# Performance work log

Hardware: AMD Instinct MI355X
Metric: run time of the kernel (lower is better)

Reference implementation:

```python
import jax, jax.numpy as jnp
import numpy as np

N, E, G, D, C = 100000, 1600000, 128, 64, 10  # nodes, edges, graphs, feat dim, classes


def setup_inputs() -> dict:
    key = jax.random.key(0)
    ks = jax.random.split(key, 14)
    s = 0.05
    return {
        "x": jax.random.normal(ks[0], (N, D), jnp.float32),
        # edge update MLP: concat(h_src,h_dst) -> hidden -> message (dim D to allow u_mul_e)
        "We1": jax.random.normal(ks[1], (2 * D, D), jnp.float32) * s,
        "be1": jnp.zeros((D,), jnp.float32),
        "We2": jax.random.normal(ks[2], (D, D), jnp.float32) * s,
        "be2": jnp.zeros((D,), jnp.float32),
        # node update MLP (hidden_dim -> hidden_dim)
        "Wn": jax.random.normal(ks[3], (D, D), jnp.float32) * s,
        "bn": jnp.zeros((D,), jnp.float32),
        # attention-pooling gate Linear(hidden_dim, 1)
        "Wg": jax.random.normal(ks[4], (D, 1), jnp.float32) * s,
        "bg": jnp.zeros((1,), jnp.float32),
        # final classifier
        "Wfc": jax.random.normal(ks[5], (D, C), jnp.float32) * s,
        "bfc": jnp.zeros((C,), jnp.float32),
        # graph structure
        "src": jax.random.randint(ks[6], (E,), 0, N),
        "dst": jax.random.randint(ks[7], (E,), 0, N),
        "graph_ids": jnp.sort(jax.random.randint(ks[8], (N,), 0, G)),
    }


def reference(x, We1, be1, We2, be2, Wn, bn, Wg, bg, Wfc, bfc, src, dst, graph_ids):
    h = x  # [N, D]
    # apply_edges: edge MLP on (h_src, h_dst) -> message m per edge  [E, D]
    e_in = jnp.concatenate([h[src], h[dst]], axis=-1)  # [E, 2D]
    m = jax.nn.relu(e_in @ We1 + be1) @ We2 + be2
    # update_all: u_mul_e('h','m') then sum-reduce onto destination nodes
    h_neigh = jax.ops.segment_sum(h[src] * m, dst, num_segments=N)  # [N, D]
    # apply_nodes: node MLP
    h2 = jax.nn.relu(h_neigh @ Wn + bn)  # [N, D]
    # GlobalAttentionPooling: per-graph softmax over node gates, weighted sum
    gate = h2 @ Wg + bg  # [N, 1]
    gmax = jax.ops.segment_max(gate, graph_ids, num_segments=G)  # [G, 1]
    a = jnp.exp(gate - gmax[graph_ids])
    denom = jax.ops.segment_sum(a, graph_ids, num_segments=G)  # [G, 1]
    a = a / denom[graph_ids]
    pooled = jax.ops.segment_sum(a * h2, graph_ids, num_segments=G)  # [G, D]
    return pooled @ Wfc + bfc  # [G, C]
```

## Files before the change

kernel.cpp:

```cpp
#include <hip/hip_runtime.h>
#include <hip/hip_bf16.h>

#define D 64
#define BSH 6
#define BNODES 64
#define NBMAX 2048
#define EB 4096

typedef _Float16 f16;
typedef _Float16 f16x4 __attribute__((ext_vector_type(4)));
typedef _Float16 f16x8 __attribute__((ext_vector_type(8)));
typedef float f32x4 __attribute__((ext_vector_type(4)));

__device__ __forceinline__ int sw7(int m, int k) {
    return (m << 7) + (((k >> 3) ^ (m & 7)) << 3) + (k & 7);
}
__device__ __forceinline__ int sw6(int m, int k) {
    return (m << 6) + ((((k >> 3) ^ (m & 7)) & 7) << 3) + (k & 7);
}

__global__ __launch_bounds__(256) void bucket_hist(
    const int* __restrict__ dst, int* __restrict__ bhist, int E, int NB)
{
    __shared__ int lhist[NBMAX];
    int tid = threadIdx.x;
    for (int b = tid; b < NB; b += 256) lhist[b] = 0;
    __syncthreads();
    int base = blockIdx.x * EB;
#pragma unroll
    for (int r = 0; r < EB / 256; ++r) {
        int e = base + r * 256 + tid;
        if (e < E) atomicAdd(&lhist[dst[e] >> BSH], 1);
    }
    __syncthreads();
    for (int b = tid; b < NB; b += 256) {
        int v = lhist[b];
        if (v) atomicAdd(&bhist[b], v);
    }
}

__global__ __launch_bounds__(256) void bucket_scan(
    const int* __restrict__ bhist, int* __restrict__ boff,
    int* __restrict__ bcursor, int NB)
{
    __shared__ int lds[256];
    int tid = threadIdx.x;
    int chunk = (NB + 255) / 256;
    int b0 = tid * chunk;
    int b1 = min(b0 + chunk, NB);
    int s = 0;
    for (int b = b0; b < b1; ++b) s += bhist[b];
    lds[tid] = s;
    __syncthreads();
    for (int d2 = 1; d2 < 256; d2 <<= 1) {
        int v = (tid >= d2) ? lds[tid - d2] : 0;
        __syncthreads();
        lds[tid] += v;
        __syncthreads();
    }
    int run = (tid == 0) ? 0 : lds[tid - 1];
    for (int b = b0; b < b1; ++b) {
        boff[b] = run;
        bcursor[b] = run;
        run += bhist[b];
    }
    if (tid == 255) boff[NB] = lds[255];
}

__global__ __launch_bounds__(256) void bucket_fill(
    const int* __restrict__ dst, const int* __restrict__ src,
    int* __restrict__ bcursor, int2* __restrict__ eix, int E, int NB)
{
    __shared__ int lhist[NBMAX];
    __shared__ int lcur[NBMAX];
    int tid = threadIdx.x;
    for (int b = tid; b < NB; b += 256) lhist[b] = 0;
    __syncthreads();
    int base = blockIdx.x * EB;
    int dv[EB / 256];
#pragma unroll
    for (int r = 0; r < EB / 256; ++r) {
        int e = base + r * 256 + tid;
        dv[r] = (e < E) ? dst[e] : -1;
        if (dv[r] >= 0) atomicAdd(&lhist[dv[r] >> BSH], 1);
    }
    __syncthreads();
    for (int b = tid; b < NB; b += 256) {
        int v = lhist[b];
        lcur[b] = v ? atomicAdd(&bcursor[b], v) : 0;
    }
    __syncthreads();
#pragma unroll
    for (int r = 0; r < EB / 256; ++r) {
        int e = base + r * 256 + tid;
        if (dv[r] >= 0) {
            int p = atomicAdd(&lcur[dv[r] >> BSH], 1);
            eix[p] = make_int2(src[e], dv[r]);
        }
    }
}

__global__ __launch_bounds__(256) void bucket_sort(
    const int2* __restrict__ eix, const int* __restrict__ boff,
    int2* __restrict__ eix2, int NB)
{
    __shared__ int h64[BNODES];
    __shared__ int cur64[BNODES];
    int bk = blockIdx.x;
    int s = boff[bk], e = boff[bk + 1];
    int tid = threadIdx.x;
    int nbase = bk << BSH;

    if (tid < BNODES) h64[tid] = 0;
    __syncthreads();
    for (int i = s + tid; i < e; i += 256)
        atomicAdd(&h64[eix[i].y - nbase], 1);
    __syncthreads();
    if (tid < BNODES) {
        int v = h64[tid];
        int inc = v;
        for (int d2 = 1; d2 < BNODES; d2 <<= 1) {
            int t = __shfl_up(inc, d2);
            if (tid >= d2) inc += t;
        }
        cur64[tid] = inc - v;
    }
    __syncthreads();
    for (int i = s + tid; i < e; i += 256) {
        int2 ed = eix[i];
        int slot = atomicAdd(&cur64[ed.y - nbase], 1);
        eix2[s + slot] = ed;
    }
}

__global__ __launch_bounds__(256, 2) void edge_mfma_kernel(
    const float* __restrict__ x,
    const float* __restrict__ We1, const float* __restrict__ be1,
    const float* __restrict__ We2, const float* __restrict__ be2,
    const int2* __restrict__ eix,
    float* __restrict__ hneigh, int N, int E, int T)
{
    __shared__ __attribute__((aligned(16))) float XCs[4][16 * 68];
    __shared__ __attribute__((aligned(16))) f16   Hbs[4][16 * 64];
    __shared__ int edsts[4][16];

    const int tid  = threadIdx.x;
    const int w    = tid >> 6;
    const int lane = tid & 63;
    const int l15  = lane & 15;
    const int quad = lane >> 4;

    float* XC  = XCs[w];
    f16*   Hb  = Hbs[w];
    int*   edst = edsts[w];

    f16x8 wb1[4][4];
#pragma unroll
    for (int kt = 0; kt < 4; ++kt)
#pragma unroll
        for (int nf = 0; nf < 4; ++nf) {
            int n = nf * 16 + l15;
#pragma unroll
            for (int j = 0; j < 8; ++j)
                wb1[kt][nf][j] = (f16)We1[(kt * 32 + quad * 8 + j) * 64 + n];
        }
    f16x8 wb2[2][4];
#pragma unroll
    for (int kt = 0; kt < 2; ++kt)
#pragma unroll
        for (int nf = 0; nf < 4; ++nf) {
            int n = nf * 16 + l15;
#pragma unroll
            for (int j = 0; j < 8; ++j)
                wb2[kt][nf][j] = (f16)We2[(kt * 32 + quad * 8 + j) * 64 + n];
        }

    float b1v[4], b2v[4];
#pragma unroll
    for (int nf = 0; nf < 4; ++nf) {
        b1v[nf] = be1[nf * 16 + l15];
        b2v[nf] = be2[nf * 16 + l15];
    }

    const int wid = blockIdx.x * 4 + w;
    const int nw  = gridDim.x * 4;

    int2 peC = eix[min(wid * 16 + l15, E - 1)];
    float4 s0, s1, s2, s3, d0v, d1v, d2v, d3v;
    {
        const float* ps = x + (size_t)peC.x * D;
        const float* pd = x + (size_t)peC.y * D;
        s0  = *(const float4*)(ps + quad * 8);
        s1  = *(const float4*)(ps + quad * 8 + 4);
        s2  = *(const float4*)(ps + 32 + quad * 8);
        s3  = *(const float4*)(ps + 32 + quad * 8 + 4);
        d0v = *(const float4*)(pd + quad * 8);
        d1v = *(const float4*)(pd + quad * 8 + 4);
        d2v = *(const float4*)(pd + 32 + quad * 8);
        d3v = *(const float4*)(pd + 32 + quad * 8 + 4);
    }
    int2 peN = eix[min((wid + nw) * 16 + l15, E - 1)];

    for (int tile = wid; tile < T; tile += nw) {
        const int e0 = tile * 16;

        int prevD = (e0 > 0)      ? eix[e0 - 1].y  : -2;
        int nextD = (e0 + 16 < E) ? eix[e0 + 16].y : -2;

        *(float4*)&XC[l15 * 68 + quad * 8]          = s0;
        *(float4*)&XC[l15 * 68 + quad * 8 + 4]      = s1;
        *(float4*)&XC[l15 * 68 + 32 + quad * 8]     = s2;
        *(float4*)&XC[l15 * 68 + 32 + quad * 8 + 4] = s3;
        if (quad == 0) edst[l15] = (e0 + l15 < E) ? peC.y : N;

        f16x8 ah[4];
        ah[0][0]=(f16)s0.x; ah[0][1]=(f16)s0.y; ah[0][2]=(f16)s0.z; ah[0][3]=(f16)s0.w;
        ah[0][4]=(f16)s1.x; ah[0][5]=(f16)s1.y; ah[0][6]=(f16)s1.z; ah[0][7]=(f16)s1.w;
        ah[1][0]=(f16)s2.x; ah[1][1]=(f16)s2.y; ah[1][2]=(f16)s2.z; ah[1][3]=(f16)s2.w;
        ah[1][4]=(f16)s3.x; ah[1][5]=(f16)s3.y; ah[1][6]=(f16)s3.z; ah[1][7]=(f16)s3.w;
        ah[2][0]=(f16)d0v.x; ah[2][1]=(f16)d0v.y; ah[2][2]=(f16)d0v.z; ah[2][3]=(f16)d0v.w;
        ah[2][4]=(f16)d1v.x; ah[2][5]=(f16)d1v.y; ah[2][6]=(f16)d1v.z; ah[2][7]=(f16)d1v.w;
        ah[3][0]=(f16)d2v.x; ah[3][1]=(f16)d2v.y; ah[3][2]=(f16)d2v.z; ah[3][3]=(f16)d2v.w;
        ah[3][4]=(f16)d3v.x; ah[3][5]=(f16)d3v.y; ah[3][6]=(f16)d3v.z; ah[3][7]=(f16)d3v.w;

        float4 t0, t1, t2, t3, u0, u1, u2, u3;
        int2 peN2;
        {
            const float* ps2 = x + (size_t)peN.x * D;
            const float* pd2 = x + (size_t)peN.y * D;
            t0 = *(const float4*)(ps2 + quad * 8);
            t1 = *(const float4*)(ps2 + quad * 8 + 4);
            t2 = *(const float4*)(ps2 + 32 + quad * 8);
            t3 = *(const float4*)(ps2 + 32 + quad * 8 + 4);
            u0 = *(const float4*)(pd2 + quad * 8);
            u1 = *(const float4*)(pd2 + quad * 8 + 4);
            u2 = *(const float4*)(pd2 + 32 + quad * 8);
            u3 = *(const float4*)(pd2 + 32 + quad * 8 + 4);
            peN2 = eix[min((tile + 2 * nw) * 16 + l15, E - 1)];
        }

        f32x4 acc[4] = {{0.f,0.f,0.f,0.f},{0.f,0.f,0.f,0.f},
                        {0.f,0.f,0.f,0.f},{0.f,0.f,0.f,0.f}};
#pragma unroll
        for (int kt = 0; kt < 4; ++kt)
#pragma unroll
            for (int nf = 0; nf < 4; ++nf)
                acc[nf] = __builtin_amdgcn_mfma_f32_16x16x32_f16(
                    ah[kt], wb1[kt][nf], acc[nf], 0, 0, 0);

#pragma unroll
        for (int nf = 0; nf < 4; ++nf)
#pragma unroll
            for (int i2 = 0; i2 < 4; ++i2)
                Hb[sw6(quad * 4 + i2, nf * 16 + l15)] =
                    (f16)fmaxf(acc[nf][i2] + b1v[nf], 0.f);

        f32x4 dd[4] = {{0.f,0.f,0.f,0.f},{0.f,0.f,0.f,0.f},
                       {0.f,0.f,0.f,0.f},{0.f,0.f,0.f,0.f}};
#pragma unroll
        for (int kt = 0; kt < 2; ++kt) {
            f16x8 ah2 = *(const f16x8*)&Hb[sw6(l15, kt * 32 + quad * 8)];
#pragma unroll
            for (int nf = 0; nf < 4; ++nf)
                dd[nf] = __builtin_amdgcn_mfma_f32_16x16x32_f16(
                    ah2, wb2[kt][nf], dd[nf], 0, 0, 0);
        }

#pragma unroll
        for (int nf = 0; nf < 4; ++nf)
#pragma unroll
            for (int i2 = 0; i2 < 4; ++i2) {
                int a = (quad * 4 + i2) * 68 + nf * 16 + l15;
                XC[a] = (dd[nf][i2] + b2v[nf]) * XC[a];
            }

        {
            int j = lane;
            float a = 0.f;
            int cur = edst[0];
            int runStart = 0;
#pragma unroll
            for (int ii = 0; ii < 16; ++ii) {
                a += XC[ii * 68 + j];
                int nxt = (ii < 15) ? edst[ii + 1] : -3;
                if (nxt != cur) {
                    bool firstRun = (runStart == 0);
                    bool lastRun = (ii == 15) || (nxt >= N);
                    bool complete = (!firstRun || prevD != cur) &&
                                    (!lastRun || nextD != cur);
                    if (complete) hneigh[(size_t)cur * D + j] = a;
                    else atomicAdd(&hneigh[(size_t)cur * D + j], a);
                    a = 0.f; cur = nxt; runStart = ii + 1;
                }
            }
        }

        s0 = t0; s1 = t1; s2 = t2; s3 = t3;
        d0v = u0; d1v = u1; d2v = u2; d3v = u3;
        peC = peN; peN = peN2;
    }
}

__global__ __launch_bounds__(256, 4) void node_mfma_kernel(
    float* __restrict__ h,
    const float* __restrict__ Wn, const float* __restrict__ bn,
    const float* __restrict__ Wg, const float* __restrict__ bg,
    float* __restrict__ gate, int N, int T)
{
    __shared__ __attribute__((aligned(16))) f16 ANhi[64 * 64];
    __shared__ __attribute__((aligned(16))) f16 ANlo[64 * 64];

    const int tid = threadIdx.x;
    const int w = tid >> 6;
    const int lane = tid & 63;
    const int l15 = lane & 15;
    const int quad = lane >> 4;
    const int m0 = w * 16;

    f16x8 wn[2][4];
#pragma unroll
    for (int kt = 0; kt < 2; ++kt)
#pragma unroll
        for (int nf = 0; nf < 4; ++nf) {
            int n = nf * 16 + l15;
#pragma unroll
            for (int j = 0; j < 8; ++j)
                wn[kt][nf][j] = (f16)Wn[(kt * 32 + quad * 8 + j) * 64 + n];
        }

    float bnv[4], wgv[4];
#pragma unroll
    for (int nt = 0; nt < 4; ++nt) {
        bnv[nt] = bn[nt * 16 + l15];
        wgv[nt] = Wg[nt * 16 + l15];
    }
    const float bgv = bg[0];

    for (int tile = blockIdx.x; tile < T; tile += gridDim.x) {
        const int t0 = tile * 64;

        {
            int i = tid >> 2;
            int q = tid & 3;
            int node = min(t0 + i, N - 1);
            const float* p = h + (size_t)node * D + q * 16;
#pragma unroll
            for (int r = 0; r < 4; ++r) {
                float4 v = *(const float4*)(p + r * 4);
                int k = q * 16 + r * 4;
                f16x4 hv, lv;
                hv[0] = (f16)v.x; lv[0] = (f16)(v.x - (float)hv[0]);
                hv[1] = (f16)v.y; lv[1] = (f16)(v.y - (float)hv[1]);
                hv[2] = (f16)v.z; lv[2] = (f16)(v.z - (float)hv[2]);
                hv[3] = (f16)v.w; lv[3] = (f16)(v.w - (float)hv[3]);
                *(f16x4*)&ANhi[sw6(i, k)] = hv;
                *(f16x4*)&ANlo[sw6(i, k)] = lv;
            }
        }
        __syncthreads();

        f32x4 cacc[4] = {{0.f,0.f,0.f,0.f},{0.f,0.f,0.f,0.f},{0.f,0.f,0.f,0.f},{0.f,0.f,0.f,0.f}};
#pragma unroll
        for (int kt = 0; kt < 2; ++kt) {
            int k = kt * 32 + quad * 8;
            f16x8 ah = *(const f16x8*)&ANhi[sw6(m0 + l15, k)];
            f16x8 al = *(const f16x8*)&ANlo[sw6(m0 + l15, k)];
#pragma unroll
            for (int nf = 0; nf < 4; ++nf) {
                cacc[nf] = __builtin_amdgcn_mfma_f32_16x16x32_f16(ah, wn[kt][nf], cacc[nf], 0, 0, 0);
                cacc[nf] = __builtin_amdgcn_mfma_f32_16x16x32_f16(al, wn[kt][nf], cacc[nf], 0, 0, 0);
            }
        }
        __syncthreads();

        float gpart[4] = {0.f, 0.f, 0.f, 0.f};
#pragma unroll
        for (int nt = 0; nt < 4; ++nt) {
            int n = nt * 16 + l15;
#pragma unroll
            for (int i2 = 0; i2 < 4; ++i2) {
                int m = t0 + m0 + quad * 4 + i2;
                float v = fmaxf(cacc[nt][i2] + bnv[nt], 0.f);
                if (m < N) h[(size_t)m * D + n] = v;
                gpart[i2] += v * wgv[nt];
            }
        }
#pragma unroll
        for (int s = 1; s < 16; s <<= 1) {
#pragma unroll
            for (int i2 = 0; i2 < 4; ++i2) gpart[i2] += __shfl_xor(gpart[i2], s);
        }
        if (l15 == 0) {
#pragma unroll
            for (int i2 = 0; i2 < 4; ++i2) {
                int m = t0 + m0 + quad * 4 + i2;
                if (m < N) gate[m] = gpart[i2] + bgv;
            }
        }
    }
}

__global__ __launch_bounds__(256) void pool_kernel(
    const float* __restrict__ h2,
    const float* __restrict__ gate,
    const int* __restrict__ gid,
    const float* __restrict__ Wfc, const float* __restrict__ bfc,
    float* __restrict__ out, int N, int C)
{
    int g = blockIdx.x;
    int tid = threadIdx.x;

    int lo = 0, hi = N;
    while (lo < hi) { int mid = (lo + hi) >> 1; if (gid[mid] < g) lo = mid + 1; else hi = mid; }
    int s = lo;
    hi = N;
    while (lo < hi) { int mid = (lo + hi) >> 1; if (gid[mid] < g + 1) lo = mid + 1; else hi = mid; }
    int e = lo;

    __shared__ float red[256];
    __shared__ float accs[4][D];
    __shared__ float dens[4];

    float m = -INFINITY;
    for (int i = s + tid; i < e; i += 256) m = fmaxf(m, gate[i]);
    red[tid] = m;
    __syncthreads();
    for (int w = 128; w > 0; w >>= 1) {
        if (tid < w) red[tid] = fmaxf(red[tid], red[tid + w]);
        __syncthreads();
    }
    float gmax = red[0];
    __syncthreads();

    int f = tid & (D - 1);
    int grp = tid >> 6;
    float acc = 0.0f, den = 0.0f;
    for (int i = s + grp; i < e; i += 4) {
        float w = expf(gate[i] - gmax);
        acc += w * h2[(size_t)i * D + f];
        if (f == 0) den += w;
    }
    accs[grp][f] = acc;
    if (f == 0) dens[grp] = den;
    __syncthreads();

    if (tid < D) {
        float p = accs[0][tid] + accs[1][tid] + accs[2][tid] + accs[3][tid];
        float dn = dens[0] + dens[1] + dens[2] + dens[3];
        p = (e > s) ? (p / dn) : 0.0f;
        red[tid] = p;
    }
    __syncthreads();

    if (tid < C) {
        float o = bfc[tid];
#pragma unroll
        for (int k = 0; k < D; ++k) o += red[k] * Wfc[k * C + tid];
        out[g * C + tid] = o;
    }
}

extern "C" void kernel_launch(void* const* d_in, const int* in_sizes, int n_in,
                              void* d_out, int out_size, void* d_ws, size_t ws_size,
                              hipStream_t stream) {
    const float* x   = (const float*)d_in[0];
    const float* We1 = (const float*)d_in[1];
    const float* be1 = (const float*)d_in[2];
    const float* We2 = (const float*)d_in[3];
    const float* be2 = (const float*)d_in[4];
    const float* Wn  = (const float*)d_in[5];
    const float* bn  = (const float*)d_in[6];
    const float* Wg  = (const float*)d_in[7];
    const float* bg  = (const float*)d_in[8];
    const float* Wfc = (const float*)d_in[9];
    const float* bfc = (const float*)d_in[10];
    const int* src = (const int*)d_in[11];
    const int* dst = (const int*)d_in[12];
    const int* gid = (const int*)d_in[13];

    const int N = in_sizes[0] / D;
    const int E = in_sizes[11];
    const int C = 10;
    const int G = out_size / C;
    const int NB = (N + BNODES - 1) / BNODES;

    int2*  eix2   = (int2*)d_ws;
    int2*  eixA   = eix2 + E;
    float* hneigh = (float*)eixA;
    float* gate   = hneigh + (size_t)(N + 1) * D;
    int*   bhist  = (int*)(gate + N);
    int*   boff   = bhist + NB;
    int*   bcursor= boff + NB + 1;
    float* outp   = (float*)d_out;

    const int Bh = (E + EB - 1) / EB;
    const int Te = (E + 15) / 16;
    const int Tn = (N + 63) / 64;

    hipMemsetAsync(bhist, 0, (size_t)NB * sizeof(int), stream);

    bucket_hist<<<Bh, 256, 0, stream>>>(dst, bhist, E, NB);
    bucket_scan<<<1, 256, 0, stream>>>(bhist, boff, bcursor, NB);
    bucket_fill<<<Bh, 256, 0, stream>>>(dst, src, bcursor, eixA, E, NB);
    bucket_sort<<<NB, 256, 0, stream>>>(eixA, boff, eix2, NB);

    hipMemsetAsync(hneigh, 0, (size_t)(N + 1) * D * sizeof(float), stream);

    edge_mfma_kernel<<<512, 256, 0, stream>>>(x, We1, be1, We2, be2,
                                              eix2, hneigh, N, E, Te);
    node_mfma_kernel<<<1024, 256, 0, stream>>>(hneigh, Wn, bn, Wg, bg, gate, N, Tn);
    pool_kernel<<<G, 256, 0, stream>>>(hneigh, gate, gid, Wfc, bfc, outp, N, C);
}
```

Before: 384.9 us.

## Fuse bucket histogram, scan and fill into one cooperative kernel

Merges the three bucketing kernels into a single cooperative launch that uses grid-wide syncs between the histogram, the scan and the fill phases. Each block keeps its local histogram and dst values across phases, so dst is read once and two launches go away. The pool kernel's weighted-sum loop is also unrolled by two with separate accumulators, and the node kernel grid is now sized to the tile count. The cooperative launch needs every block (about 391) to be resident at once, and the serial single-block scan now holds the whole grid at a barrier.

```diff
diff --git a/kernel.cpp b/kernel.cpp
--- a/kernel.cpp
+++ b/kernel.cpp
@@ -1,5 +1,8 @@
 #include <hip/hip_runtime.h>
 #include <hip/hip_bf16.h>
+#include <hip/hip_cooperative_groups.h>
+
+namespace cg = cooperative_groups;
 
 #define D 64
 #define BSH 6
@@ -12,70 +15,24 @@
 typedef _Float16 f16x8 __attribute__((ext_vector_type(8)));
 typedef float f32x4 __attribute__((ext_vector_type(4)));
 
-__device__ __forceinline__ int sw7(int m, int k) {
-    return (m << 7) + (((k >> 3) ^ (m & 7)) << 3) + (k & 7);
-}
 __device__ __forceinline__ int sw6(int m, int k) {
     return (m << 6) + ((((k >> 3) ^ (m & 7)) & 7) << 3) + (k & 7);
 }
 
-__global__ __launch_bounds__(256) void bucket_hist(
-    const int* __restrict__ dst, int* __restrict__ bhist, int E, int NB)
+__global__ __launch_bounds__(256) void bucket_prep(
+    const int* __restrict__ dst, const int* __restrict__ src,
+    int* __restrict__ bhist, int* __restrict__ boff,
+    int* __restrict__ bcursor, int2* __restrict__ eixA, int E, int NB)
 {
+    cg::grid_group grid = cg::this_grid();
     __shared__ int lhist[NBMAX];
+    __shared__ int lcur[NBMAX];
+    __shared__ int sscan[256];
+
     int tid = threadIdx.x;
     for (int b = tid; b < NB; b += 256) lhist[b] = 0;
     __syncthreads();
-    int base = blockIdx.x * EB;
-#pragma unroll
-    for (int r = 0; r < EB / 256; ++r) {
-        int e = base + r * 256 + tid;
-        if (e < E) atomicAdd(&lhist[dst[e] >> BSH], 1);
-    }
-    __syncthreads();
-    for (int b = tid; b < NB; b += 256) {
-        int v = lhist[b];
-        if (v) atomicAdd(&bhist[b], v);
-    }
-}
-
-__global__ __launch_bounds__(256) void bucket_scan(
-    const int* __restrict__ bhist, int* __restrict__ boff,
-    int* __restrict__ bcursor, int NB)
-{
-    __shared__ int lds[256];
-    int tid = threadIdx.x;
-    int chunk = (NB + 255) / 256;
-    int b0 = tid * chunk;
-    int b1 = min(b0 + chunk, NB);
-    int s = 0;
-    for (int b = b0; b < b1; ++b) s += bhist[b];
-    lds[tid] = s;
-    __syncthreads();
-    for (int d2 = 1; d2 < 256; d2 <<= 1) {
-        int v = (tid >= d2) ? lds[tid - d2] : 0;
-        __syncthreads();
-        lds[tid] += v;
-        __syncthreads();
-    }
-    int run = (tid == 0) ? 0 : lds[tid - 1];
-    for (int b = b0; b < b1; ++b) {
-        boff[b] = run;
-        bcursor[b] = run;
-        run += bhist[b];
-    }
-    if (tid == 255) boff[NB] = lds[255];
-}
-
-__global__ __launch_bounds__(256) void bucket_fill(
-    const int* __restrict__ dst, const int* __restrict__ src,
-    int* __restrict__ bcursor, int2* __restrict__ eix, int E, int NB)
-{
-    __shared__ int lhist[NBMAX];
-    __shared__ int lcur[NBMAX];
-    int tid = threadIdx.x;
-    for (int b = tid; b < NB; b += 256) lhist[b] = 0;
-    __syncthreads();
+
     int base = blockIdx.x * EB;
     int dv[EB / 256];
 #pragma unroll
@@ -87,6 +44,36 @@
     __syncthreads();
     for (int b = tid; b < NB; b += 256) {
         int v = lhist[b];
+        if (v) atomicAdd(&bhist[b], v);
+    }
+    grid.sync();
+
+    if (blockIdx.x == 0) {
+        int chunk = (NB + 255) / 256;
+        int b0 = tid * chunk;
+        int b1 = min(b0 + chunk, NB);
+        int s = 0;
+        for (int b = b0; b < b1; ++b) s += bhist[b];
+        sscan[tid] = s;
+        __syncthreads();
+        for (int d2 = 1; d2 < 256; d2 <<= 1) {
+            int v = (tid >= d2) ? sscan[tid - d2] : 0;
+            __syncthreads();
+            sscan[tid] += v;
+            __syncthreads();
+        }
+        int run = (tid == 0) ? 0 : sscan[tid - 1];
+        for (int b = b0; b < b1; ++b) {
+            boff[b] = run;
+            bcursor[b] = run;
+            run += bhist[b];
+        }
+        if (tid == 255) boff[NB] = sscan[255];
+    }
+    grid.sync();
+
+    for (int b = tid; b < NB; b += 256) {
+        int v = lhist[b];
         lcur[b] = v ? atomicAdd(&bcursor[b], v) : 0;
     }
     __syncthreads();
@@ -95,7 +82,7 @@
         int e = base + r * 256 + tid;
         if (dv[r] >= 0) {
             int p = atomicAdd(&lcur[dv[r] >> BSH], 1);
-            eix[p] = make_int2(src[e], dv[r]);
+            eixA[p] = make_int2(src[e], dv[r]);
         }
     }
 }
@@ -434,14 +421,22 @@
 
     int f = tid & (D - 1);
     int grp = tid >> 6;
-    float acc = 0.0f, den = 0.0f;
-    for (int i = s + grp; i < e; i += 4) {
-        float w = expf(gate[i] - gmax);
-        acc += w * h2[(size_t)i * D + f];
-        if (f == 0) den += w;
-    }
-    accs[grp][f] = acc;
-    if (f == 0) dens[grp] = den;
+    float acc0 = 0.0f, den0 = 0.0f, acc1 = 0.0f, den1 = 0.0f;
+    int i = s + grp;
+    for (; i + 4 < e; i += 8) {
+        float w0 = expf(gate[i] - gmax);
+        float w1 = expf(gate[i + 4] - gmax);
+        acc0 += w0 * h2[(size_t)i * D + f];
+        acc1 += w1 * h2[(size_t)(i + 4) * D + f];
+        if (f == 0) { den0 += w0; den1 += w1; }
+    }
+    for (; i < e; i += 4) {
+        float w0 = expf(gate[i] - gmax);
+        acc0 += w0 * h2[(size_t)i * D + f];
+        if (f == 0) den0 += w0;
+    }
+    accs[grp][f] = acc0 + acc1;
+    if (f == 0) dens[grp] = den0 + den1;
     __syncthreads();
 
     if (tid < D) {
@@ -499,15 +494,22 @@
 
     hipMemsetAsync(bhist, 0, (size_t)NB * sizeof(int), stream);
 
-    bucket_hist<<<Bh, 256, 0, stream>>>(dst, bhist, E, NB);
-    bucket_scan<<<1, 256, 0, stream>>>(bhist, boff, bcursor, NB);
-    bucket_fill<<<Bh, 256, 0, stream>>>(dst, src, bcursor, eixA, E, NB);
+    {
+        const int* dst_a = dst;
+        const int* src_a = src;
+        int E_a = E, NB_a = NB;
+        void* args[] = {(void*)&dst_a, (void*)&src_a, (void*)&bhist,
+                        (void*)&boff, (void*)&bcursor, (void*)&eixA,
+                        (void*)&E_a, (void*)&NB_a};
+        hipLaunchCooperativeKernel((const void*)bucket_prep,
+                                   dim3(Bh), dim3(256), args, 0, stream);
+    }
     bucket_sort<<<NB, 256, 0, stream>>>(eixA, boff, eix2, NB);
 
     hipMemsetAsync(hneigh, 0, (size_t)(N + 1) * D * sizeof(float), stream);
 
     edge_mfma_kernel<<<512, 256, 0, stream>>>(x, We1, be1, We2, be2,
                                               eix2, hneigh, N, E, Te);
-    node_mfma_kernel<<<1024, 256, 0, stream>>>(hneigh, Wn, bn, Wg, bg, gate, N, Tn);
+    node_mfma_kernel<<<Tn, 256, 0, stream>>>(hneigh, Wn, bn, Wg, bg, gate, N, Tn);
     pool_kernel<<<G, 256, 0, stream>>>(hneigh, gate, gid, Wfc, bfc, outp, N, C);
 }
```

After: 459.6 us. 19.4% more time.

## Split attention pooling per graph into partial blocks with log-sum-exp combine

Applied to the files above, without the earlier changes.

The pooling stage is split into a partial kernel that runs PPARTS blocks per graph, each computing a local max, exp-sum and weighted feature sum over its slice of nodes. A second small kernel rescales the partials with the global max, normalises, and applies the classifier. The goal is more parallelism than one block per graph across 128 graphs, at the cost of an extra launch and a reused workspace region.

```diff
diff --git a/kernel.cpp b/kernel.cpp
--- a/kernel.cpp
+++ b/kernel.cpp
@@ -6,15 +6,13 @@
 #define BNODES 64
 #define NBMAX 2048
 #define EB 4096
+#define PPARTS 4
 
 typedef _Float16 f16;
 typedef _Float16 f16x4 __attribute__((ext_vector_type(4)));
 typedef _Float16 f16x8 __attribute__((ext_vector_type(8)));
 typedef float f32x4 __attribute__((ext_vector_type(4)));
 
-__device__ __forceinline__ int sw7(int m, int k) {
-    return (m << 7) + (((k >> 3) ^ (m & 7)) << 3) + (k & 7);
-}
 __device__ __forceinline__ int sw6(int m, int k) {
     return (m << 6) + ((((k >> 3) ^ (m & 7)) & 7) << 3) + (k & 7);
 }
@@ -400,14 +398,16 @@
     }
 }
 
-__global__ __launch_bounds__(256) void pool_kernel(
+__global__ __launch_bounds__(256) void pool_partial(
     const float* __restrict__ h2,
     const float* __restrict__ gate,
     const int* __restrict__ gid,
-    const float* __restrict__ Wfc, const float* __restrict__ bfc,
-    float* __restrict__ out, int N, int C)
-{
-    int g = blockIdx.x;
+    float* __restrict__ pm, float* __restrict__ pden,
+    float* __restrict__ pacc, int N)
+{
+    int gb = blockIdx.x;
+    int g = gb / PPARTS;
+    int p = gb % PPARTS;
     int tid = threadIdx.x;
 
     int lo = 0, hi = N;
@@ -417,39 +417,70 @@
     while (lo < hi) { int mid = (lo + hi) >> 1; if (gid[mid] < g + 1) lo = mid + 1; else hi = mid; }
     int e = lo;
 
+    int len = e - s;
+    int st = s + (int)(((long long)len * p) / PPARTS);
+    int en = s + (int)(((long long)len * (p + 1)) / PPARTS);
+
     __shared__ float red[256];
     __shared__ float accs[4][D];
     __shared__ float dens[4];
 
     float m = -INFINITY;
-    for (int i = s + tid; i < e; i += 256) m = fmaxf(m, gate[i]);
+    for (int i = st + tid; i < en; i += 256) m = fmaxf(m, gate[i]);
     red[tid] = m;
     __syncthreads();
     for (int w = 128; w > 0; w >>= 1) {
         if (tid < w) red[tid] = fmaxf(red[tid], red[tid + w]);
         __syncthreads();
     }
-    float gmax = red[0];
+    float lmax = red[0];
     __syncthreads();
 
     int f = tid & (D - 1);
     int grp = tid >> 6;
     float acc = 0.0f, den = 0.0f;
-    for (int i = s + grp; i < e; i += 4) {
-        float w = expf(gate[i] - gmax);
-        acc += w * h2[(size_t)i * D + f];
-        if (f == 0) den += w;
+    for (int i = st + grp; i < en; i += 4) {
+        float wv = expf(gate[i] - lmax);
+        acc += wv * h2[(size_t)i * D + f];
+        if (f == 0) den += wv;
     }
     accs[grp][f] = acc;
     if (f == 0) dens[grp] = den;
     __syncthreads();
 
-    if (tid < D) {
-        float p = accs[0][tid] + accs[1][tid] + accs[2][tid] + accs[3][tid];
-        float dn = dens[0] + dens[1] + dens[2] + dens[3];
-        p = (e > s) ? (p / dn) : 0.0f;
-        red[tid] = p;
-    }
+    if (tid < D)
+        pacc[(size_t)gb * D + tid] =
+            accs[0][tid] + accs[1][tid] + accs[2][tid] + accs[3][tid];
+    if (tid == 0) {
+        pden[gb] = dens[0] + dens[1] + dens[2] + dens[3];
+        pm[gb] = lmax;
+    }
+}
+
+__global__ __launch_bounds__(64) void pool_combine(
+    const float* __restrict__ pm, const float* __restrict__ pden,
+    const float* __restrict__ pacc,
+    const float* __restrict__ Wfc, const float* __restrict__ bfc,
+    float* __restrict__ out, int C)
+{
+    int g = blockIdx.x;
+    int tid = threadIdx.x;
+
+    __shared__ float red[D];
+
+    float m = -INFINITY;
+#pragma unroll
+    for (int p = 0; p < PPARTS; ++p) m = fmaxf(m, pm[g * PPARTS + p]);
+
+    float den = 0.f, pf = 0.f;
+#pragma unroll
+    for (int p = 0; p < PPARTS; ++p) {
+        float mp = pm[g * PPARTS + p];
+        float sc = (mp > -INFINITY) ? expf(mp - m) : 0.f;
+        den += pden[g * PPARTS + p] * sc;
+        pf  += pacc[(size_t)(g * PPARTS + p) * D + tid] * sc;
+    }
+    red[tid] = (den > 0.f) ? (pf / den) : 0.f;
     __syncthreads();
 
     if (tid < C) {
@@ -493,6 +524,10 @@
     int*   bcursor= boff + NB + 1;
     float* outp   = (float*)d_out;
 
+    float* pm   = (float*)eix2;
+    float* pden = pm + (size_t)G * PPARTS;
+    float* pacc = pden + (size_t)G * PPARTS;
+
     const int Bh = (E + EB - 1) / EB;
     const int Te = (E + 15) / 16;
     const int Tn = (N + 63) / 64;
@@ -509,5 +544,7 @@
     edge_mfma_kernel<<<512, 256, 0, stream>>>(x, We1, be1, We2, be2,
                                               eix2, hneigh, N, E, Te);
     node_mfma_kernel<<<1024, 256, 0, stream>>>(hneigh, Wn, bn, Wg, bg, gate, N, Tn);
-    pool_kernel<<<G, 256, 0, stream>>>(hneigh, gate, gid, Wfc, bfc, outp, N, C);
-}
+    pool_partial<<<G * PPARTS, 256, 0, stream>>>(hneigh, gate, gid,
+                                                 pm, pden, pacc, N);
+    pool_combine<<<G, 64, 0, stream>>>(pm, pden, pacc, Wfc, bfc, outp, C);
+}
```

Result: faster. 350.6 us (-8.9%).
